# Performance work log

Measured on AMD Instinct MI355X. Metric: run time of the kernel, lower is better.

The kernel has to match this reference:

```python
import jax, jax.numpy as jnp
import numpy as np

IN_F, OUT_F, GROUP = 4096, 11008, 128

# NF4 codebook (normalized-float-4 levels), matches NF4_LEVELS in the source
NF4_LEVELS = jnp.array([
    -1.0, -0.6961928009986877, -0.5250730514526367, -0.39491748809814453,
    -0.28444138169288635, -0.18477343022823334, -0.09105003625154495, 0.0,
    0.07958029955625534, 0.16093020141124725, 0.24611230194568634,
    0.33791524171829224, 0.44070982933044434, 0.5626170039176941,
    0.7229568362236023, 1.0], dtype=jnp.float32)


def setup_inputs() -> dict:
    key = jax.random.key(0)
    k0, k1, k2, k3 = jax.random.split(key, 4)
    x = jax.random.normal(k0, (32, 1, IN_F), dtype=jnp.float32)
    # one int32 per packed byte; low nibble = even element code, high nibble = odd
    packed = jax.random.randint(k1, (OUT_F * IN_F // 2,), 0, 256, dtype=jnp.int32)
    # per-group absmax scales (positive)
    scales = jax.random.uniform(k2, (OUT_F * IN_F // GROUP,), dtype=jnp.float32) * 0.02 + 1e-4
    bias_param = jax.random.normal(k3, (OUT_F,), dtype=jnp.float32)
    return {"x": x, "packed": packed, "scales": scales, "bias_param": bias_param}


def dequant_nf4(packed, scales):
    # unpack two 4-bit codes per byte; interleave as quantized[0::2]=low, [1::2]=high
    low = packed & 15
    high = (packed >> 4) & 15
    codes = jnp.stack([low, high], axis=-1).reshape(-1)          # [OUT_F*IN_F]
    vals = NF4_LEVELS[codes]                                      # codebook lookup
    w = (vals.reshape(-1, GROUP) * scales[:, None]).reshape(OUT_F, IN_F)
    return w


def reference(x, packed, scales, bias_param):
    W = dequant_nf4(packed, scales)                               # [OUT_F, IN_F]
    # y = x @ W^T + b  (F.linear semantics)
    return jnp.einsum('bsi,oi->bso', x, W) + bias_param
```

## Files before the change

kernel.cpp:

```cpp
#include <hip/hip_runtime.h>
#include <hip/hip_bf16.h>

#define IN_F   4096
#define OUT_F  11008
#define BATCH  32
#define NTILE  64
#define KSPLIT 4
#define GRID_N (OUT_F / NTILE)

typedef __attribute__((ext_vector_type(8))) short  bf16x8;
typedef __attribute__((ext_vector_type(4))) float  f32x4;
typedef __attribute__((ext_vector_type(4))) int    i32x4;
typedef __attribute__((ext_vector_type(4))) float  float4v;

static __device__ __constant__ float NF4_LEVELS[16] = {
    -1.0f, -0.6961928009986877f, -0.5250730514526367f, -0.39491748809814453f,
    -0.28444138169288635f, -0.18477343022823334f, -0.09105003625154495f, 0.0f,
    0.07958029955625534f, 0.16093020141124725f, 0.24611230194568634f,
    0.33791524171829224f, 0.44070982933044434f, 0.5626170039176941f,
    0.7229568362236023f, 1.0f};

__global__ void prelude_kernel(const float* __restrict__ x,
                               const float* __restrict__ bias,
                               unsigned short* __restrict__ frag,
                               float* __restrict__ out) {
    const int bid = blockIdx.x, tid = threadIdx.x;
    if (bid < 64) {
        int T  = bid * 256 + tid;
        int st = T >> 13;
        int kb = (T >> 6) & 127;
        int l  = T & 63;
        int row = st * 16 + (l & 15);
        int k0  = kb * 32 + (l >> 4) * 8;
        const float* src = x + (size_t)row * IN_F + k0;
        unsigned w[4];
        #pragma unroll
        for (int e = 0; e < 4; ++e) {
            unsigned lo = __builtin_bit_cast(unsigned short, __float2bfloat16(src[2 * e]));
            unsigned hi = __builtin_bit_cast(unsigned short, __float2bfloat16(src[2 * e + 1]));
            w[e] = lo | (hi << 16);
        }
        i32x4 v = { (int)w[0], (int)w[1], (int)w[2], (int)w[3] };
        *reinterpret_cast<i32x4*>(frag + ((size_t)st * 8192 + kb * 64 + l) * 8) = v;
    } else {
        int t2 = (bid - 64) * 256 + tid;
        int i  = t2 * 4;
        int o  = i % OUT_F;
        float4v b = *reinterpret_cast<const float4v*>(bias + o);
        *reinterpret_cast<float4v*>(out + i) = b;
    }
}

__global__ __launch_bounds__(256, 4) void nf4_gemm_kernel(
        const int* __restrict__ packed,
        const float* __restrict__ scales,
        const unsigned short* __restrict__ frag,
        float* __restrict__ out)
{
    __shared__ unsigned lds[9216];

    const int tid  = threadIdx.x;
    const int wave = tid >> 6;
    const int lane = tid & 63;
    const int col  = lane & 15;
    const int g    = lane >> 4;

    const int n0 = blockIdx.x * NTILE;
    const int by = blockIdx.y;

    #pragma unroll
    for (int q = 0; q < 4; ++q) {
        int e = q * 64 + lane;
        unsigned lo = __builtin_bit_cast(unsigned short, __float2bfloat16(NF4_LEVELS[e & 15]));
        unsigned hi = __builtin_bit_cast(unsigned short, __float2bfloat16(NF4_LEVELS[(e >> 4) & 15]));
        lds[wave * 256 + e] = lo | (hi << 16);
    }

    float2 scp[4];
    #pragma unroll
    for (int st = 0; st < 4; ++st)
        scp[st] = *reinterpret_cast<const float2*>(
            scales + (size_t)(n0 + st * 16 + col) * 32 + by * 8 + wave * 2);

    #define SLOAD(bb, sr)                                                      \
        _Pragma("unroll")                                                      \
        for (int ii = 0; ii < 8; ++ii) {                                       \
            int row = (bb) * 16 + 2 * ii + (lane >> 5);                        \
            sr[ii] = *reinterpret_cast<const i32x4*>(                          \
                packed + (size_t)(n0 + row) * (IN_F / 2)                       \
                       + by * 512 + wave * 128 + (lane & 31) * 4);             \
        }

    #define SWRITE(bb, sr)                                                     \
        _Pragma("unroll")                                                      \
        for (int ii = 0; ii < 8; ++ii) {                                       \
            int row = (bb) * 16 + 2 * ii + (lane >> 5);                        \
            int j   = lane & 31;                                               \
            int d   = (j & 0x10) | ((j & 3) << 2) | ((j >> 2) & 3);            \
            unsigned v = ((unsigned)(sr[ii][0] & 255))                         \
                       | ((unsigned)(sr[ii][1] & 255) << 8)                    \
                       | ((unsigned)(sr[ii][2] & 255) << 16)                   \
                       | ((unsigned)(sr[ii][3] & 255) << 24);                  \
            lds[1024 + wave * 2048 + ((row * 32 + d) ^ ((row & 7) << 2))] = v; \
        }

    {
        i32x4 sa[8], sb[8];
        SLOAD(0, sa) SLOAD(1, sb) SWRITE(0, sa)
        SLOAD(2, sa) SWRITE(1, sb)
        SLOAD(3, sb) SWRITE(2, sa) SWRITE(3, sb)
    }

    f32x4 acc[4][2];
    #pragma unroll
    for (int st = 0; st < 4; ++st) {
        acc[st][0] = (f32x4){0.f,0.f,0.f,0.f};
        acc[st][1] = (f32x4){0.f,0.f,0.f,0.f};
    }

    const unsigned short* f0 = frag;
    const unsigned short* f1 = frag + 65536;

    #pragma unroll
    for (int grp = 0; grp < 2; ++grp) {
        bf16x8 A0[4], A1[4];
        #pragma unroll
        for (int t = 0; t < 4; ++t) {
            int kb = by * 32 + wave * 8 + grp * 4 + t;
            A0[t] = *reinterpret_cast<const bf16x8*>(f0 + ((size_t)kb * 64 + lane) * 8);
            A1[t] = *reinterpret_cast<const bf16x8*>(f1 + ((size_t)kb * 64 + lane) * 8);
        }
        #pragma unroll
        for (int st = 0; st < 4; ++st) {
            int row = st * 16 + col;
            i32x4 cd = *reinterpret_cast<const i32x4*>(
                &lds[1024 + wave * 2048 +
                     ((row * 32 + grp * 16 + g * 4) ^ ((row & 7) << 2))]);
            f32x4 t0 = (f32x4){0.f,0.f,0.f,0.f};
            f32x4 t1 = (f32x4){0.f,0.f,0.f,0.f};
            #pragma unroll
            for (int t = 0; t < 4; ++t) {
                unsigned code = (unsigned)cd[t];
                i32x4 bu;
                bu[0] = (int)lds[wave * 256 + (code & 255u)];
                bu[1] = (int)lds[wave * 256 + ((code >> 8) & 255u)];
                bu[2] = (int)lds[wave * 256 + ((code >> 16) & 255u)];
                bu[3] = (int)lds[wave * 256 + (code >> 24)];
                bf16x8 bf = __builtin_bit_cast(bf16x8, bu);
                t0 = __builtin_amdgcn_mfma_f32_16x16x32_bf16(A0[t], bf, t0, 0, 0, 0);
                t1 = __builtin_amdgcn_mfma_f32_16x16x32_bf16(A1[t], bf, t1, 0, 0, 0);
            }
            const float sc = (grp == 0) ? scp[st].x : scp[st].y;
            #pragma unroll
            for (int j = 0; j < 4; ++j) {
                acc[st][0][j] = fmaf(sc, t0[j], acc[st][0][j]);
                acc[st][1][j] = fmaf(sc, t1[j], acc[st][1][j]);
            }
        }
    }

    float* red = (float*)&lds[1024 + wave * 2048];
    #pragma unroll
    for (int st = 0; st < 4; ++st)
        #pragma unroll
        for (int j = 0; j < 4; ++j) {
            red[(0 * 16 + g * 4 + j) * 64 + st * 16 + col] = acc[st][0][j];
            red[(1 * 16 + g * 4 + j) * 64 + st * 16 + col] = acc[st][1][j];
        }
    __syncthreads();

    const float* rbase = (const float*)&lds[1024];
    #pragma unroll
    for (int p = 0; p < 8; ++p) {
        int b = p * 4 + wave;
        float s = rbase[b * 64 + lane] + rbase[2048 + b * 64 + lane]
                + rbase[4096 + b * 64 + lane] + rbase[6144 + b * 64 + lane];
        unsafeAtomicAdd(out + (size_t)b * OUT_F + n0 + lane, s);
    }
}

extern "C" void kernel_launch(void* const* d_in, const int* in_sizes, int n_in,
                              void* d_out, int out_size, void* d_ws, size_t ws_size,
                              hipStream_t stream) {
    const float* x      = (const float*)d_in[0];
    const int*   packed = (const int*)d_in[1];
    const float* scales = (const float*)d_in[2];
    const float* bias   = (const float*)d_in[3];
    float* out = (float*)d_out;

    unsigned short* frag = (unsigned short*)d_ws;

    prelude_kernel<<<408, 256, 0, stream>>>(x, bias, frag, out);
    nf4_gemm_kernel<<<dim3(GRID_N, KSPLIT), 256, 0, stream>>>(packed, scales, frag, out);
}
```

Baseline: 29.94 us.

## Split K eight ways and give each wave its own output rows, dropping LDS reduction

Doubles the K split so the grid has twice as many blocks, and reassigns work so each wave owns 16 output columns over the block's whole K slice instead of a quarter of K across all 64 columns. This removes the cross-wave LDS reduction and its __syncthreads, and shrinks shared memory. In exchange each output element now takes twice as many global atomic adds (eight K slices instead of four), and every wave loads the same A fragments, which raises redundant activation traffic.

```diff
diff --git a/kernel.cpp b/kernel.cpp
--- a/kernel.cpp
+++ b/kernel.cpp
@@ -5,7 +5,7 @@
 #define OUT_F  11008
 #define BATCH  32
 #define NTILE  64
-#define KSPLIT 4
+#define KSPLIT 8
 #define GRID_N (OUT_F / NTILE)
 
 typedef __attribute__((ext_vector_type(8))) short  bf16x8;
@@ -57,7 +57,7 @@
         const unsigned short* __restrict__ frag,
         float* __restrict__ out)
 {
-    __shared__ unsigned lds[9216];
+    __shared__ unsigned lds[5120];
 
     const int tid  = threadIdx.x;
     const int wave = tid >> 6;
@@ -65,8 +65,9 @@
     const int col  = lane & 15;
     const int g    = lane >> 4;
 
-    const int n0 = blockIdx.x * NTILE;
-    const int by = blockIdx.y;
+    const int n0      = blockIdx.x * NTILE;
+    const int by      = blockIdx.y;
+    const int rowbase = n0 + wave * 16;
 
     #pragma unroll
     for (int q = 0; q < 4; ++q) {
@@ -76,106 +77,81 @@
         lds[wave * 256 + e] = lo | (hi << 16);
     }
 
-    float2 scp[4];
-    #pragma unroll
-    for (int st = 0; st < 4; ++st)
-        scp[st] = *reinterpret_cast<const float2*>(
-            scales + (size_t)(n0 + st * 16 + col) * 32 + by * 8 + wave * 2);
+    float4v scv = *reinterpret_cast<const float4v*>(
+        scales + (size_t)(rowbase + col) * 32 + by * 4);
+    float sca[4] = { scv.x, scv.y, scv.z, scv.w };
 
-    #define SLOAD(bb, sr)                                                      \
+    const int dperm = (lane & 0x30) | ((lane & 3) << 2) | ((lane >> 2) & 3);
+    unsigned* cbuf = &lds[1024 + wave * 1024];
+
+    #define SLOAD(r0, sr)                                                      \
         _Pragma("unroll")                                                      \
         for (int ii = 0; ii < 8; ++ii) {                                       \
-            int row = (bb) * 16 + 2 * ii + (lane >> 5);                        \
             sr[ii] = *reinterpret_cast<const i32x4*>(                          \
-                packed + (size_t)(n0 + row) * (IN_F / 2)                       \
-                       + by * 512 + wave * 128 + (lane & 31) * 4);             \
+                packed + (size_t)(rowbase + (r0) + ii) * (IN_F / 2)            \
+                       + by * 256 + lane * 4);                                 \
         }
 
-    #define SWRITE(bb, sr)                                                     \
+    #define SWRITE(r0, sr)                                                     \
         _Pragma("unroll")                                                      \
         for (int ii = 0; ii < 8; ++ii) {                                       \
-            int row = (bb) * 16 + 2 * ii + (lane >> 5);                        \
-            int j   = lane & 31;                                               \
-            int d   = (j & 0x10) | ((j & 3) << 2) | ((j >> 2) & 3);            \
+            int rl = (r0) + ii;                                                \
             unsigned v = ((unsigned)(sr[ii][0] & 255))                         \
                        | ((unsigned)(sr[ii][1] & 255) << 8)                    \
                        | ((unsigned)(sr[ii][2] & 255) << 16)                   \
-                       | ((unsigned)(sr[ii][3] & 255) << 24);                  \
-            lds[1024 + wave * 2048 + ((row * 32 + d) ^ ((row & 7) << 2))] = v; \
+                       | ((unsigned)sr[ii][3] << 24);                          \
+            cbuf[(rl * 64 + dperm) ^ ((rl & 7) << 2)] = v;                     \
         }
 
     {
-        i32x4 sa[8], sb[8];
-        SLOAD(0, sa) SLOAD(1, sb) SWRITE(0, sa)
-        SLOAD(2, sa) SWRITE(1, sb)
-        SLOAD(3, sb) SWRITE(2, sa) SWRITE(3, sb)
+        i32x4 sr[8];
+        SLOAD(0, sr) SWRITE(0, sr)
+        SLOAD(8, sr) SWRITE(8, sr)
     }
 
-    f32x4 acc[4][2];
-    #pragma unroll
-    for (int st = 0; st < 4; ++st) {
-        acc[st][0] = (f32x4){0.f,0.f,0.f,0.f};
-        acc[st][1] = (f32x4){0.f,0.f,0.f,0.f};
-    }
+    f32x4 acc0 = (f32x4){0.f,0.f,0.f,0.f};
+    f32x4 acc1 = (f32x4){0.f,0.f,0.f,0.f};
 
     const unsigned short* f0 = frag;
     const unsigned short* f1 = frag + 65536;
 
     #pragma unroll
-    for (int grp = 0; grp < 2; ++grp) {
+    for (int grp = 0; grp < 4; ++grp) {
         bf16x8 A0[4], A1[4];
         #pragma unroll
         for (int t = 0; t < 4; ++t) {
-            int kb = by * 32 + wave * 8 + grp * 4 + t;
+            int kb = by * 16 + grp * 4 + t;
             A0[t] = *reinterpret_cast<const bf16x8*>(f0 + ((size_t)kb * 64 + lane) * 8);
             A1[t] = *reinterpret_cast<const bf16x8*>(f1 + ((size_t)kb * 64 + lane) * 8);
         }
+        i32x4 cd = *reinterpret_cast<const i32x4*>(
+            &cbuf[(col * 64 + grp * 16 + g * 4) ^ ((col & 7) << 2)]);
+
+        f32x4 t0 = (f32x4){0.f,0.f,0.f,0.f};
+        f32x4 t1 = (f32x4){0.f,0.f,0.f,0.f};
         #pragma unroll
-        for (int st = 0; st < 4; ++st) {
-            int row = st * 16 + col;
-            i32x4 cd = *reinterpret_cast<const i32x4*>(
-                &lds[1024 + wave * 2048 +
-                     ((row * 32 + grp * 16 + g * 4) ^ ((row & 7) << 2))]);
-            f32x4 t0 = (f32x4){0.f,0.f,0.f,0.f};
-            f32x4 t1 = (f32x4){0.f,0.f,0.f,0.f};
-            #pragma unroll
-            for (int t = 0; t < 4; ++t) {
-                unsigned code = (unsigned)cd[t];
-                i32x4 bu;
-                bu[0] = (int)lds[wave * 256 + (code & 255u)];
-                bu[1] = (int)lds[wave * 256 + ((code >> 8) & 255u)];
-                bu[2] = (int)lds[wave * 256 + ((code >> 16) & 255u)];
-                bu[3] = (int)lds[wave * 256 + (code >> 24)];
-                bf16x8 bf = __builtin_bit_cast(bf16x8, bu);
-                t0 = __builtin_amdgcn_mfma_f32_16x16x32_bf16(A0[t], bf, t0, 0, 0, 0);
-                t1 = __builtin_amdgcn_mfma_f32_16x16x32_bf16(A1[t], bf, t1, 0, 0, 0);
-            }
-            const float sc = (grp == 0) ? scp[st].x : scp[st].y;
-            #pragma unroll
-            for (int j = 0; j < 4; ++j) {
-                acc[st][0][j] = fmaf(sc, t0[j], acc[st][0][j]);
-                acc[st][1][j] = fmaf(sc, t1[j], acc[st][1][j]);
-            }
+        for (int t = 0; t < 4; ++t) {
+            unsigned code = (unsigned)cd[t];
+            i32x4 bu;
+            bu[0] = (int)lds[wave * 256 + (code & 255u)];
+            bu[1] = (int)lds[wave * 256 + ((code >> 8) & 255u)];
+            bu[2] = (int)lds[wave * 256 + ((code >> 16) & 255u)];
+            bu[3] = (int)lds[wave * 256 + (code >> 24)];
+            bf16x8 bf = __builtin_bit_cast(bf16x8, bu);
+            t0 = __builtin_amdgcn_mfma_f32_16x16x32_bf16(A0[t], bf, t0, 0, 0, 0);
+            t1 = __builtin_amdgcn_mfma_f32_16x16x32_bf16(A1[t], bf, t1, 0, 0, 0);
+        }
+        #pragma unroll
+        for (int j = 0; j < 4; ++j) {
+            acc0[j] = fmaf(sca[grp], t0[j], acc0[j]);
+            acc1[j] = fmaf(sca[grp], t1[j], acc1[j]);
         }
     }
 
-    float* red = (float*)&lds[1024 + wave * 2048];
     #pragma unroll
-    for (int st = 0; st < 4; ++st)
-        #pragma unroll
-        for (int j = 0; j < 4; ++j) {
-            red[(0 * 16 + g * 4 + j) * 64 + st * 16 + col] = acc[st][0][j];
-            red[(1 * 16 + g * 4 + j) * 64 + st * 16 + col] = acc[st][1][j];
-        }
-    __syncthreads();
-
-    const float* rbase = (const float*)&lds[1024];
-    #pragma unroll
-    for (int p = 0; p < 8; ++p) {
-        int b = p * 4 + wave;
-        float s = rbase[b * 64 + lane] + rbase[2048 + b * 64 + lane]
-                + rbase[4096 + b * 64 + lane] + rbase[6144 + b * 64 + lane];
-        unsafeAtomicAdd(out + (size_t)b * OUT_F + n0 + lane, s);
+    for (int j = 0; j < 4; ++j) {
+        unsafeAtomicAdd(out + (size_t)(g * 4 + j) * OUT_F + rowbase + col, acc0[j]);
+        unsafeAtomicAdd(out + (size_t)(16 + g * 4 + j) * OUT_F + rowbase + col, acc1[j]);
     }
 }
 
```

New measurement: 31.27 us. 4.4% more time.
